# Performance work log

Measured on AMD Instinct MI355X. Metric: run time of the kernel, lower is better.

## Reference

```python
import jax, jax.numpy as jnp
import numpy as np

DIM = 1024
HEADS = 8
HEAD_DIM = DIM // HEADS
D_STATE = 256
BATCH = 8192
DT_MIN = 1e-3
DT_MAX = 1e-1
EPS = 1e-4  # RMSNorm eps


def setup_inputs() -> dict:
    key = jax.random.key(0)
    ks = jax.random.split(key, 8)
    x_t = jax.random.normal(ks[0], (BATCH, DIM), dtype=jnp.float32)
    state_re = jax.random.normal(ks[1], (BATCH, HEADS, D_STATE), dtype=jnp.float32)
    state_im = jax.random.normal(ks[2], (BATCH, HEADS, D_STATE), dtype=jnp.float32)
    # parameters (match torch init)
    norm_weight = jnp.ones((DIM,), dtype=jnp.float32)
    A_re_log = jnp.full((HEADS, D_STATE), float(np.log(0.5)), dtype=jnp.float32)
    n = jnp.arange(1, D_STATE + 1, dtype=jnp.float32)
    A_im = jnp.broadcast_to(float(np.pi) * n, (HEADS, D_STATE)).astype(jnp.float32)
    b_scale = 1.0 / float(np.sqrt(HEAD_DIM))
    c_scale = 1.0 / float(np.sqrt(D_STATE))
    B_re = jax.random.normal(ks[3], (HEADS, D_STATE, HEAD_DIM), dtype=jnp.float32) * b_scale
    B_im = jax.random.normal(ks[4], (HEADS, D_STATE, HEAD_DIM), dtype=jnp.float32) * b_scale
    C_re = jax.random.normal(ks[5], (HEADS, HEAD_DIM, D_STATE), dtype=jnp.float32) * c_scale
    C_im = jax.random.normal(ks[6], (HEADS, HEAD_DIM, D_STATE), dtype=jnp.float32) * c_scale
    D = jnp.ones((DIM,), dtype=jnp.float32)
    # log_dt: inverse-softplus of log-uniform dt in [dt_min, dt_max]
    u = jax.random.uniform(ks[7], (HEADS, D_STATE), dtype=jnp.float32)
    dt = jnp.exp(u * (np.log(DT_MAX) - np.log(DT_MIN)) + np.log(DT_MIN))
    dt = jnp.maximum(dt, 1e-4)
    log_dt = dt + jnp.log(-jnp.expm1(-dt))
    return dict(x_t=x_t, state_re=state_re, state_im=state_im,
                norm_weight=norm_weight, A_re_log=A_re_log, A_im=A_im,
                B_re=B_re, B_im=B_im, C_re=C_re, C_im=C_im, D=D, log_dt=log_dt)


def reference(x_t, state_re, state_im, norm_weight, A_re_log, A_im,
              B_re, B_im, C_re, C_im, D, log_dt):
    batch = x_t.shape[0]
    # RMSNorm (eps=1e-4, elementwise affine)
    ms = jnp.mean(jnp.square(x_t), axis=-1, keepdims=True)
    x = x_t * jax.lax.rsqrt(ms + EPS) * norm_weight
    x_h = x.reshape(batch, HEADS, HEAD_DIM)  # (B,H,P)
    # discretize
    A = jax.lax.complex(-jnp.exp(A_re_log), A_im)            # (H,N)
    dt = jax.nn.softplus(log_dt)                              # (H,N)
    A_bar = jnp.exp(dt.astype(A.dtype) * A)                   # (H,N) complex
    B = jax.lax.complex(B_re, B_im)                           # (H,N,P)
    C = jax.lax.complex(C_re, C_im)                           # (H,P,N)
    B_bar = ((A_bar - 1.0) / A)[..., None] * B                # (H,N,P)
    # recurrent step
    state = jax.lax.complex(state_re, state_im)               # (B,H,N)
    Bx = jnp.einsum('hnp,bhp->bhn', B_bar, x_h.astype(B_bar.dtype))
    new_state = A_bar[None] * state + Bx                      # (B,H,N)
    Ch = jnp.einsum('hpn,bhn->bhp', C, new_state)             # (B,H,P)
    D_h = D.reshape(HEADS, HEAD_DIM)[None]                    # (1,H,P)
    y_h = 2.0 * Ch.real + D_h * x_h
    out = x_t + y_h.reshape(batch, DIM)
    return out, new_state.real, new_state.imag
```

## Files before the change

kernel.cpp:

```cpp
#include <hip/hip_runtime.h>

#define BATCH 8192
#define DIM 1024
#define HEADS 8
#define HEAD_DIM 128
#define DSTATE 256

typedef __attribute__((ext_vector_type(8))) short short8v;
typedef __attribute__((ext_vector_type(4))) float f32x4;
typedef __attribute__((ext_vector_type(4))) unsigned short ushort4v;
typedef __attribute__((ext_vector_type(4))) unsigned int uint4v;

__device__ __forceinline__ unsigned short f2bf(float x) {
  unsigned int u = __builtin_bit_cast(unsigned int, x);
  unsigned int r = u + 0x7FFFu + ((u >> 16) & 1u);
  return (unsigned short)(r >> 16);
}
__device__ __forceinline__ float bf2f(unsigned short h) {
  unsigned int u = ((unsigned int)h) << 16;
  return __builtin_bit_cast(float, u);
}

__device__ __forceinline__ void stage16f(const float* g, float* l) {
  __builtin_amdgcn_global_load_lds(
      (const __attribute__((address_space(1))) unsigned int*)g,
      (__attribute__((address_space(3))) unsigned int*)l, 16, 0, 0);
}
__device__ __forceinline__ void stage16u(const unsigned short* g, unsigned short* l) {
  __builtin_amdgcn_global_load_lds(
      (const __attribute__((address_space(1))) unsigned int*)g,
      (__attribute__((address_space(3))) unsigned int*)l, 16, 0, 0);
}

#define BARRIER() do { \
  asm volatile("s_waitcnt lgkmcnt(0)" ::: "memory"); \
  __builtin_amdgcn_s_barrier(); \
  asm volatile("" ::: "memory"); } while (0)


__global__ void pc_params(const float* __restrict__ logdt,
                          const float* __restrict__ arelog,
                          const float* __restrict__ aim,
                          float* __restrict__ abr, float* __restrict__ abi,
                          float* __restrict__ cre, float* __restrict__ cim) {
  int i = blockIdx.x * 256 + threadIdx.x;
  float ld = logdt[i];
  float dt = log1pf(expf(ld));
  float Ar = -expf(arelog[i]);
  float Ai = aim[i];
  float e  = expf(dt * Ar);
  float th = dt * Ai;
  float Abr = e * cosf(th), Abi = e * sinf(th);
  int n = i & 255, h = i >> 8;
  int s = (n & ~31) + ((n >> 2) & 1) * 16 + ((n >> 3) & 3) * 4 + (n & 3);
  abr[h * 256 + s] = Abr; abi[h * 256 + s] = Abi;
  float den = Ar * Ar + Ai * Ai;
  float br = Abr - 1.0f;
  cre[i] = (br * Ar + Abi * Ai) / den;
  cim[i] = (Abi * Ar - br * Ai) / den;
}

__global__ void pc_w1(const float* __restrict__ Bre, const float* __restrict__ Bim,
                      const float* __restrict__ cre, const float* __restrict__ cim,
                      unsigned short* __restrict__ w1re, unsigned short* __restrict__ w1im) {
  int i = blockIdx.x * 256 + threadIdx.x;
  int p = i & 127, s = (i >> 7) & 255, h = i >> 15;
  int kk = s >> 4, u = s & 15;
  int n = ((kk >> 1) << 5) + ((u >> 2) & 3) * 8 + (kk & 1) * 4 + (u & 3);
  int src = (h * 256 + n) * 128 + p;
  int hn = h * 256 + n;
  float cr = cre[hn], ci = cim[hn];
  float br = Bre[src], bi = Bim[src];
  w1re[i] = f2bf(cr * br - ci * bi);
  w1im[i] = f2bf(cr * bi + ci * br);
}

__global__ void pc_w2(const float* __restrict__ Cre, const float* __restrict__ Cim,
                      unsigned short* __restrict__ w2re, unsigned short* __restrict__ w2mi) {
  int i = blockIdx.x * 256 + threadIdx.x;
  w2re[i] = f2bf(Cre[i]);
  w2mi[i] = f2bf(-Cim[i]);
}

__global__ __launch_bounds__(256) void rms_k(const float* __restrict__ xt,
                                             const float* __restrict__ w,
                                             unsigned short* __restrict__ xbf) {
  int wid = threadIdx.x >> 6, lane = threadIdx.x & 63;
  int row = blockIdx.x * 4 + wid;
  const float* xr = xt + (long)row * DIM;
  f32x4 v[4];
  float ssq = 0.f;
  #pragma unroll
  for (int c = 0; c < 4; ++c) {
    v[c] = *(const f32x4*)(xr + c * 256 + lane * 4);
    ssq += v[c][0]*v[c][0] + v[c][1]*v[c][1] + v[c][2]*v[c][2] + v[c][3]*v[c][3];
  }
  #pragma unroll
  for (int m = 1; m < 64; m <<= 1) ssq += __shfl_xor(ssq, m, 64);
  float sc = rsqrtf(ssq * (1.0f / DIM) + 1e-4f);
  unsigned short* orow = xbf + (long)row * DIM;
  #pragma unroll
  for (int c = 0; c < 4; ++c) {
    f32x4 w4 = *(const f32x4*)(w + c * 256 + lane * 4);
    ushort4v o;
    o[0] = f2bf(v[c][0] * sc * w4[0]);
    o[1] = f2bf(v[c][1] * sc * w4[1]);
    o[2] = f2bf(v[c][2] * sc * w4[2]);
    o[3] = f2bf(v[c][3] * sc * w4[3]);
    *(ushort4v*)(orow + c * 256 + lane * 4) = o;
  }
}

__global__ __launch_bounds__(512, 2) void s5_main(
    const unsigned short* __restrict__ xbf,
    const unsigned short* __restrict__ w1re, const unsigned short* __restrict__ w1im,
    const unsigned short* __restrict__ w2re, const unsigned short* __restrict__ w2mi,
    const float* __restrict__ abrp, const float* __restrict__ abip,
    const float* __restrict__ sre, const float* __restrict__ sim,
    const float* __restrict__ xt, const float* __restrict__ dvec,
    float* __restrict__ out, float* __restrict__ nsre, float* __restrict__ nsim) {
  __shared__ float Sb[3][2][16][256];
  __shared__ float xtl[3][16][128];
  __shared__ unsigned short xbl[3][16][128];
  __shared__ unsigned short pf[2][8][64][8];
  const int tid = threadIdx.x;
  const int w = tid >> 6, lane = tid & 63;
  const int g = lane >> 4, bl = lane & 15;
  const int h = blockIdx.x & 7;
  const int blkrow = (blockIdx.x >> 3) * 256;

  short8v w1r[2][4], w1i[2][4];
  #pragma unroll
  for (int t = 0; t < 2; ++t) {
    const int kk = 2 * w + t;
    const unsigned short* pr = w1re + ((size_t)(h * DSTATE + kk * 16 + bl)) * HEAD_DIM + g * 8;
    const unsigned short* pi = w1im + ((size_t)(h * DSTATE + kk * 16 + bl)) * HEAD_DIM + g * 8;
    #pragma unroll
    for (int ks = 0; ks < 4; ++ks) {
      w1r[t][ks] = *(const short8v*)(pr + ks * 32);
      w1i[t][ks] = *(const short8v*)(pi + ks * 32);
    }
  }
  short8v w2r[8], w2i[8];
  {
    const unsigned short* qr = w2re + ((size_t)(h * HEAD_DIM + w * 16 + bl)) * DSTATE + g * 8;
    const unsigned short* qi = w2mi + ((size_t)(h * HEAD_DIM + w * 16 + bl)) * DSTATE + g * 8;
    #pragma unroll
    for (int j = 0; j < 8; ++j) {
      w2r[j] = *(const short8v*)(qr + j * 32);
      w2i[j] = *(const short8v*)(qi + j * 32);
    }
  }
  f32x4 Arh[2], Aih[2];
  #pragma unroll
  for (int t = 0; t < 2; ++t) {
    Arh[t] = *(const f32x4*)(abrp + h * DSTATE + (2 * w + t) * 16 + g * 4);
    Aih[t] = *(const f32x4*)(abip + h * DSTATE + (2 * w + t) * 16 + g * 4);
  }
  const f32x4 d4 = *(const f32x4*)(dvec + h * HEAD_DIM + w * 16 + g * 4);

  auto STAGE = [&](int t, int b3) {
    const int gr0 = blkrow + t * 16;
    #pragma unroll
    for (int i = 0; i < 2; ++i) {
      const int row = 2 * w + i;
      const size_t rb = ((size_t)(gr0 + row) * HEADS + h) * DSTATE;
      const int soff = (lane ^ (row & 7)) * 4;
      stage16f(sre + rb + soff, &Sb[b3][0][row][0]);
      stage16f(sim + rb + soff, &Sb[b3][1][row][0]);
    }
    {
      const int row = 2 * w + (lane >> 5);
      const float* src = xt + (size_t)(gr0 + row) * DIM + h * HEAD_DIM + (lane & 31) * 4;
      stage16f(src, &xtl[b3][2 * w][0]);
    }
    if (w < 4) {
      const int row = 4 * w + (lane >> 4);
      const unsigned short* src = xbf + (size_t)(gr0 + row) * DIM + h * HEAD_DIM + (lane & 15) * 8;
      stage16u(src, &xbl[b3][4 * w][0]);
    }
  };

  STAGE(0, 0);
  asm volatile("s_waitcnt vmcnt(0)" ::: "memory");
  __builtin_amdgcn_s_barrier();
  asm volatile("" ::: "memory");

  int bcur = 0;
  for (int t = 0; t < 16; ++t) {
    const int bnxt = (bcur == 2) ? 0 : bcur + 1;
    if (t < 15) {
      STAGE(t + 1, bnxt);
      asm volatile("s_waitcnt vmcnt(6)" ::: "memory");
    } else {
      asm volatile("s_waitcnt vmcnt(0)" ::: "memory");
    }
    BARRIER();

    short8v xf[4];
    #pragma unroll
    for (int ks = 0; ks < 4; ++ks)
      xf[ks] = *(const short8v*)&xbl[bcur][bl][ks * 32 + g * 8];

    unsigned pr0 = 0, pr1 = 0, pi0 = 0, pi1 = 0;
    #pragma unroll
    for (int tt = 0; tt < 2; ++tt) {
      f32x4 dr = {0.f,0.f,0.f,0.f};
      f32x4 di = {0.f,0.f,0.f,0.f};
      #pragma unroll
      for (int ks = 0; ks < 4; ++ks)
        dr = __builtin_amdgcn_mfma_f32_16x16x32_bf16(w1r[tt][ks], xf[ks], dr, 0, 0, 0);
      #pragma unroll
      for (int ks = 0; ks < 4; ++ks)
        di = __builtin_amdgcn_mfma_f32_16x16x32_bf16(w1i[tt][ks], xf[ks], di, 0, 0, 0);
      const int c = (((8 * w + 2 * g + tt) ^ (bl & 7)) << 2);
      const f32x4 s_r = *(const f32x4*)&Sb[bcur][0][bl][c];
      const f32x4 s_i = *(const f32x4*)&Sb[bcur][1][bl][c];
      f32x4 nr, ni;
      #pragma unroll
      for (int r = 0; r < 4; ++r) {
        nr[r] = fmaf(Arh[tt][r], s_r[r], fmaf(-Aih[tt][r], s_i[r], dr[r]));
        ni[r] = fmaf(Arh[tt][r], s_i[r], fmaf(Aih[tt][r], s_r[r], di[r]));
      }
      *(f32x4*)&Sb[bcur][0][bl][c] = nr;
      *(f32x4*)&Sb[bcur][1][bl][c] = ni;
      unsigned lo  = (unsigned)f2bf(nr[0]) | ((unsigned)f2bf(nr[1]) << 16);
      unsigned hi  = (unsigned)f2bf(nr[2]) | ((unsigned)f2bf(nr[3]) << 16);
      unsigned lo2 = (unsigned)f2bf(ni[0]) | ((unsigned)f2bf(ni[1]) << 16);
      unsigned hi2 = (unsigned)f2bf(ni[2]) | ((unsigned)f2bf(ni[3]) << 16);
      if (tt == 0) { pr0 = lo; pr1 = hi; pi0 = lo2; pi1 = hi2; }
      else {
        uint4v urv; urv[0] = pr0; urv[1] = pr1; urv[2] = lo;  urv[3] = hi;
        uint4v uiv; uiv[0] = pi0; uiv[1] = pi1; uiv[2] = lo2; uiv[3] = hi2;
        *(short8v*)&pf[0][w][lane][0] = __builtin_bit_cast(short8v, urv);
        *(short8v*)&pf[1][w][lane][0] = __builtin_bit_cast(short8v, uiv);
      }
    }
    BARRIER();

    #pragma unroll
    for (int i = 0; i < 2; ++i) {
      const int row = 2 * w + i;
      const size_t rb = ((size_t)(blkrow + t * 16 + row) * HEADS + h) * DSTATE;
      const int gc = (lane ^ (row & 7)) * 4;
      const f32x4 vr = *(const f32x4*)&Sb[bcur][0][row][lane * 4];
      const f32x4 vi = *(const f32x4*)&Sb[bcur][1][row][lane * 4];
      *(f32x4*)(nsre + rb + gc) = vr;
      *(f32x4*)(nsim + rb + gc) = vi;
    }

    f32x4 a2 = {0.f,0.f,0.f,0.f};
    #pragma unroll
    for (int j = 0; j < 8; ++j) {
      const short8v pbr = *(const short8v*)&pf[0][j][lane][0];
      const short8v pbi = *(const short8v*)&pf[1][j][lane][0];
      a2 = __builtin_amdgcn_mfma_f32_16x16x32_bf16(w2r[j], pbr, a2, 0, 0, 0);
      a2 = __builtin_amdgcn_mfma_f32_16x16x32_bf16(w2i[j], pbi, a2, 0, 0, 0);
    }

    {
      const int col = h * HEAD_DIM + w * 16 + g * 4;
      const size_t o = (size_t)(blkrow + t * 16 + bl) * DIM + col;
      const f32x4 xt4 = *(const f32x4*)&xtl[bcur][bl][w * 16 + g * 4];
      const ushort4v xh4 = *(const ushort4v*)&xbl[bcur][bl][w * 16 + g * 4];
      f32x4 ro;
      #pragma unroll
      for (int r = 0; r < 4; ++r)
        ro[r] = xt4[r] + 2.0f * a2[r] + d4[r] * bf2f(xh4[r]);
      *(f32x4*)(out + o) = ro;
    }
    bcur = bnxt;
  }
}

extern "C" void kernel_launch(void* const* d_in, const int* in_sizes, int n_in,
                              void* d_out, int out_size, void* d_ws, size_t ws_size,
                              hipStream_t stream) {
  const float* x_t      = (const float*)d_in[0];
  const float* state_re = (const float*)d_in[1];
  const float* state_im = (const float*)d_in[2];
  const float* norm_w   = (const float*)d_in[3];
  const float* A_re_log = (const float*)d_in[4];
  const float* A_im     = (const float*)d_in[5];
  const float* B_re     = (const float*)d_in[6];
  const float* B_im     = (const float*)d_in[7];
  const float* C_re     = (const float*)d_in[8];
  const float* C_im     = (const float*)d_in[9];
  const float* Dv       = (const float*)d_in[10];
  const float* log_dt   = (const float*)d_in[11];

  float* out   = (float*)d_out;
  float* ns_re = out + (size_t)BATCH * DIM;
  float* ns_im = ns_re + (size_t)BATCH * HEADS * DSTATE;

  char* ws = (char*)d_ws;
  unsigned short* xbf  = (unsigned short*)ws;
  unsigned short* w1re = (unsigned short*)(ws + 16777216);
  unsigned short* w1im = w1re + 262144;
  unsigned short* w2re = w1im + 262144;
  unsigned short* w2mi = w2re + 262144;
  float* abr = (float*)(ws + 16777216 + 4 * 524288);
  float* abi = abr + 2048;
  float* cre = abi + 2048;
  float* cim = cre + 2048;

  pc_params<<<8, 256, 0, stream>>>(log_dt, A_re_log, A_im, abr, abi, cre, cim);
  pc_w1<<<1024, 256, 0, stream>>>(B_re, B_im, cre, cim, w1re, w1im);
  pc_w2<<<1024, 256, 0, stream>>>(C_re, C_im, w2re, w2mi);
  rms_k<<<2048, 256, 0, stream>>>(x_t, norm_w, xbf);
  s5_main<<<256, 512, 0, stream>>>(xbf, w1re, w1im, w2re, w2mi, abr, abi,
                                   state_re, state_im, x_t, Dv, out, ns_re, ns_im);
}
```

Before: 101.1 us.

## Fuse prep kernels, fold RMSNorm scale into main kernel, deepen staging pipeline

Result: faster. 92.30 us (-8.7%).

```diff
diff --git a/kernel.cpp b/kernel.cpp
--- a/kernel.cpp
+++ b/kernel.cpp
@@ -26,10 +26,10 @@
       (const __attribute__((address_space(1))) unsigned int*)g,
       (__attribute__((address_space(3))) unsigned int*)l, 16, 0, 0);
 }
-__device__ __forceinline__ void stage16u(const unsigned short* g, unsigned short* l) {
+__device__ __forceinline__ void stage4f(const float* g, float* l) {
   __builtin_amdgcn_global_load_lds(
       (const __attribute__((address_space(1))) unsigned int*)g,
-      (__attribute__((address_space(3))) unsigned int*)l, 16, 0, 0);
+      (__attribute__((address_space(3))) unsigned int*)l, 4, 0, 0);
 }
 
 #define BARRIER() do { \
@@ -38,91 +38,72 @@
   asm volatile("" ::: "memory"); } while (0)
 
 
-__global__ void pc_params(const float* __restrict__ logdt,
-                          const float* __restrict__ arelog,
-                          const float* __restrict__ aim,
-                          float* __restrict__ abr, float* __restrict__ abi,
-                          float* __restrict__ cre, float* __restrict__ cim) {
-  int i = blockIdx.x * 256 + threadIdx.x;
-  float ld = logdt[i];
-  float dt = log1pf(expf(ld));
-  float Ar = -expf(arelog[i]);
-  float Ai = aim[i];
-  float e  = expf(dt * Ar);
-  float th = dt * Ai;
-  float Abr = e * cosf(th), Abi = e * sinf(th);
-  int n = i & 255, h = i >> 8;
-  int s = (n & ~31) + ((n >> 2) & 1) * 16 + ((n >> 3) & 3) * 4 + (n & 3);
-  abr[h * 256 + s] = Abr; abi[h * 256 + s] = Abi;
-  float den = Ar * Ar + Ai * Ai;
-  float br = Abr - 1.0f;
-  cre[i] = (br * Ar + Abi * Ai) / den;
-  cim[i] = (Abi * Ar - br * Ai) / den;
-}
-
-__global__ void pc_w1(const float* __restrict__ Bre, const float* __restrict__ Bim,
-                      const float* __restrict__ cre, const float* __restrict__ cim,
-                      unsigned short* __restrict__ w1re, unsigned short* __restrict__ w1im) {
-  int i = blockIdx.x * 256 + threadIdx.x;
-  int p = i & 127, s = (i >> 7) & 255, h = i >> 15;
-  int kk = s >> 4, u = s & 15;
-  int n = ((kk >> 1) << 5) + ((u >> 2) & 3) * 8 + (kk & 1) * 4 + (u & 3);
-  int src = (h * 256 + n) * 128 + p;
-  int hn = h * 256 + n;
-  float cr = cre[hn], ci = cim[hn];
-  float br = Bre[src], bi = Bim[src];
-  w1re[i] = f2bf(cr * br - ci * bi);
-  w1im[i] = f2bf(cr * bi + ci * br);
-}
-
-__global__ void pc_w2(const float* __restrict__ Cre, const float* __restrict__ Cim,
-                      unsigned short* __restrict__ w2re, unsigned short* __restrict__ w2mi) {
-  int i = blockIdx.x * 256 + threadIdx.x;
-  w2re[i] = f2bf(Cre[i]);
-  w2mi[i] = f2bf(-Cim[i]);
-}
-
-__global__ __launch_bounds__(256) void rms_k(const float* __restrict__ xt,
-                                             const float* __restrict__ w,
-                                             unsigned short* __restrict__ xbf) {
-  int wid = threadIdx.x >> 6, lane = threadIdx.x & 63;
-  int row = blockIdx.x * 4 + wid;
-  const float* xr = xt + (long)row * DIM;
-  f32x4 v[4];
-  float ssq = 0.f;
-  #pragma unroll
-  for (int c = 0; c < 4; ++c) {
-    v[c] = *(const f32x4*)(xr + c * 256 + lane * 4);
-    ssq += v[c][0]*v[c][0] + v[c][1]*v[c][1] + v[c][2]*v[c][2] + v[c][3]*v[c][3];
-  }
-  #pragma unroll
-  for (int m = 1; m < 64; m <<= 1) ssq += __shfl_xor(ssq, m, 64);
-  float sc = rsqrtf(ssq * (1.0f / DIM) + 1e-4f);
-  unsigned short* orow = xbf + (long)row * DIM;
-  #pragma unroll
-  for (int c = 0; c < 4; ++c) {
-    f32x4 w4 = *(const f32x4*)(w + c * 256 + lane * 4);
-    ushort4v o;
-    o[0] = f2bf(v[c][0] * sc * w4[0]);
-    o[1] = f2bf(v[c][1] * sc * w4[1]);
-    o[2] = f2bf(v[c][2] * sc * w4[2]);
-    o[3] = f2bf(v[c][3] * sc * w4[3]);
-    *(ushort4v*)(orow + c * 256 + lane * 4) = o;
+__global__ __launch_bounds__(256) void prep(
+    const float* __restrict__ logdt, const float* __restrict__ arelog,
+    const float* __restrict__ aim,
+    const float* __restrict__ Bre, const float* __restrict__ Bim,
+    const float* __restrict__ Cre, const float* __restrict__ Cim,
+    const float* __restrict__ xtg, const float* __restrict__ normw,
+    unsigned short* __restrict__ w1re, unsigned short* __restrict__ w1im,
+    unsigned short* __restrict__ w2re, unsigned short* __restrict__ w2mi,
+    float* __restrict__ abr, float* __restrict__ abi,
+    float* __restrict__ scale) {
+  const int blk = blockIdx.x;
+  if (blk < 1024) {
+    const int i = blk * 256 + threadIdx.x;
+    const int p = i & 127, s = (i >> 7) & 255, h = i >> 15;
+    const int kk = s >> 4, u = s & 15;
+    const int n = ((kk >> 1) << 5) + ((u >> 2) & 3) * 8 + (kk & 1) * 4 + (u & 3);
+    const int hn = h * 256 + n;
+    const float ld = logdt[hn];
+    const float dt = log1pf(expf(ld));
+    const float Ar = -expf(arelog[hn]);
+    const float Ai = aim[hn];
+    const float e = expf(dt * Ar), th = dt * Ai;
+    const float Abr = e * cosf(th), Abi = e * sinf(th);
+    if (p == 0) { abr[h * 256 + s] = Abr; abi[h * 256 + s] = Abi; }
+    const float den = Ar * Ar + Ai * Ai;
+    const float br_ = Abr - 1.0f;
+    const float cr = (br_ * Ar + Abi * Ai) / den;
+    const float ci = (Abi * Ar - br_ * Ai) / den;
+    const int src = hn * 128 + p;
+    const float wb = normw[h * 128 + p];
+    const float bre = Bre[src], bim = Bim[src];
+    w1re[i] = f2bf((cr * bre - ci * bim) * wb);
+    w1im[i] = f2bf((cr * bim + ci * bre) * wb);
+  } else if (blk < 2048) {
+    const int i = (blk - 1024) * 256 + threadIdx.x;
+    w2re[i] = f2bf(Cre[i]);
+    w2mi[i] = f2bf(-Cim[i]);
+  } else {
+    const int wid = threadIdx.x >> 6, lane = threadIdx.x & 63;
+    const int row = (blk - 2048) * 4 + wid;
+    const float* xr = xtg + (size_t)row * DIM;
+    float ssq = 0.f;
+    #pragma unroll
+    for (int c = 0; c < 4; ++c) {
+      const f32x4 v = *(const f32x4*)(xr + c * 256 + lane * 4);
+      ssq += v[0]*v[0] + v[1]*v[1] + v[2]*v[2] + v[3]*v[3];
+    }
+    #pragma unroll
+    for (int m = 1; m < 64; m <<= 1) ssq += __shfl_xor(ssq, m, 64);
+    if (lane == 0) scale[row] = rsqrtf(ssq * (1.0f / DIM) + 1e-4f);
   }
 }
 
 __global__ __launch_bounds__(512, 2) void s5_main(
-    const unsigned short* __restrict__ xbf,
     const unsigned short* __restrict__ w1re, const unsigned short* __restrict__ w1im,
     const unsigned short* __restrict__ w2re, const unsigned short* __restrict__ w2mi,
     const float* __restrict__ abrp, const float* __restrict__ abip,
+    const float* __restrict__ scale,
     const float* __restrict__ sre, const float* __restrict__ sim,
     const float* __restrict__ xt, const float* __restrict__ dvec,
+    const float* __restrict__ normw,
     float* __restrict__ out, float* __restrict__ nsre, float* __restrict__ nsim) {
   __shared__ float Sb[3][2][16][256];
   __shared__ float xtl[3][16][128];
-  __shared__ unsigned short xbl[3][16][128];
   __shared__ unsigned short pf[2][8][64][8];
+  __shared__ float scL[3][64];
   const int tid = threadIdx.x;
   const int w = tid >> 6, lane = tid & 63;
   const int g = lane >> 4, bl = lane & 15;
@@ -157,7 +138,14 @@
     Arh[t] = *(const f32x4*)(abrp + h * DSTATE + (2 * w + t) * 16 + g * 4);
     Aih[t] = *(const f32x4*)(abip + h * DSTATE + (2 * w + t) * 16 + g * 4);
   }
-  const f32x4 d4 = *(const f32x4*)(dvec + h * HEAD_DIM + w * 16 + g * 4);
+  f32x4 d4;
+  {
+    const int col = h * HEAD_DIM + w * 16 + g * 4;
+    const f32x4 dv = *(const f32x4*)(dvec + col);
+    const f32x4 nv = *(const f32x4*)(normw + col);
+    #pragma unroll
+    for (int r = 0; r < 4; ++r) d4[r] = dv[r] * nv[r];
+  }
 
   auto STAGE = [&](int t, int b3) {
     const int gr0 = blkrow + t * 16;
@@ -171,36 +159,37 @@
     }
     {
       const int row = 2 * w + (lane >> 5);
-      const float* src = xt + (size_t)(gr0 + row) * DIM + h * HEAD_DIM + (lane & 31) * 4;
+      const int soff = ((lane & 31) ^ (row & 7)) * 4;
+      const float* src = xt + (size_t)(gr0 + row) * DIM + h * HEAD_DIM + soff;
       stage16f(src, &xtl[b3][2 * w][0]);
     }
-    if (w < 4) {
-      const int row = 4 * w + (lane >> 4);
-      const unsigned short* src = xbf + (size_t)(gr0 + row) * DIM + h * HEAD_DIM + (lane & 15) * 8;
-      stage16u(src, &xbl[b3][4 * w][0]);
-    }
+    stage4f(scale + gr0 + (lane & 15), &scL[b3][0]);
   };
 
   STAGE(0, 0);
-  asm volatile("s_waitcnt vmcnt(0)" ::: "memory");
-  __builtin_amdgcn_s_barrier();
-  asm volatile("" ::: "memory");
-
-  int bcur = 0;
+  STAGE(1, 1);
+
   for (int t = 0; t < 16; ++t) {
-    const int bnxt = (bcur == 2) ? 0 : bcur + 1;
-    if (t < 15) {
-      STAGE(t + 1, bnxt);
-      asm volatile("s_waitcnt vmcnt(6)" ::: "memory");
-    } else {
-      asm volatile("s_waitcnt vmcnt(0)" ::: "memory");
-    }
+    const int bcur = t % 3;
+    if (t < 2) { asm volatile("s_waitcnt vmcnt(6)"  ::: "memory"); }
+    else       { asm volatile("s_waitcnt vmcnt(10)" ::: "memory"); }
     BARRIER();
 
+    if (t + 2 < 16) STAGE(t + 2, (t + 2) % 3);
+
+    const float scl = scL[bcur][bl];
     short8v xf[4];
     #pragma unroll
-    for (int ks = 0; ks < 4; ++ks)
-      xf[ks] = *(const short8v*)&xbl[bcur][bl][ks * 32 + g * 8];
+    for (int ks = 0; ks < 4; ++ks) {
+      const f32x4 x0 = *(const f32x4*)&xtl[bcur][bl][(((ks * 8 + 2 * g)     ^ (bl & 7)) << 2)];
+      const f32x4 x1 = *(const f32x4*)&xtl[bcur][bl][(((ks * 8 + 2 * g + 1) ^ (bl & 7)) << 2)];
+      uint4v uv;
+      uv[0] = (unsigned)f2bf(x0[0] * scl) | ((unsigned)f2bf(x0[1] * scl) << 16);
+      uv[1] = (unsigned)f2bf(x0[2] * scl) | ((unsigned)f2bf(x0[3] * scl) << 16);
+      uv[2] = (unsigned)f2bf(x1[0] * scl) | ((unsigned)f2bf(x1[1] * scl) << 16);
+      uv[3] = (unsigned)f2bf(x1[2] * scl) | ((unsigned)f2bf(x1[3] * scl) << 16);
+      xf[ks] = __builtin_bit_cast(short8v, uv);
+    }
 
     unsigned pr0 = 0, pr1 = 0, pi0 = 0, pi1 = 0;
     #pragma unroll
@@ -261,15 +250,13 @@
     {
       const int col = h * HEAD_DIM + w * 16 + g * 4;
       const size_t o = (size_t)(blkrow + t * 16 + bl) * DIM + col;
-      const f32x4 xt4 = *(const f32x4*)&xtl[bcur][bl][w * 16 + g * 4];
-      const ushort4v xh4 = *(const ushort4v*)&xbl[bcur][bl][w * 16 + g * 4];
+      const f32x4 xt4 = *(const f32x4*)&xtl[bcur][bl][(((4 * w + g) ^ (bl & 7)) << 2)];
       f32x4 ro;
       #pragma unroll
       for (int r = 0; r < 4; ++r)
-        ro[r] = xt4[r] + 2.0f * a2[r] + d4[r] * bf2f(xh4[r]);
+        ro[r] = xt4[r] * (1.0f + d4[r] * scl) + 2.0f * a2[r];
       *(f32x4*)(out + o) = ro;
     }
-    bcur = bnxt;
   }
 }
 
@@ -294,20 +281,18 @@
   float* ns_im = ns_re + (size_t)BATCH * HEADS * DSTATE;
 
   char* ws = (char*)d_ws;
-  unsigned short* xbf  = (unsigned short*)ws;
-  unsigned short* w1re = (unsigned short*)(ws + 16777216);
+  unsigned short* w1re = (unsigned short*)ws;
   unsigned short* w1im = w1re + 262144;
   unsigned short* w2re = w1im + 262144;
   unsigned short* w2mi = w2re + 262144;
-  float* abr = (float*)(ws + 16777216 + 4 * 524288);
-  float* abi = abr + 2048;
-  float* cre = abi + 2048;
-  float* cim = cre + 2048;
-
-  pc_params<<<8, 256, 0, stream>>>(log_dt, A_re_log, A_im, abr, abi, cre, cim);
-  pc_w1<<<1024, 256, 0, stream>>>(B_re, B_im, cre, cim, w1re, w1im);
-  pc_w2<<<1024, 256, 0, stream>>>(C_re, C_im, w2re, w2mi);
-  rms_k<<<2048, 256, 0, stream>>>(x_t, norm_w, xbf);
-  s5_main<<<256, 512, 0, stream>>>(xbf, w1re, w1im, w2re, w2mi, abr, abi,
-                                   state_re, state_im, x_t, Dv, out, ns_re, ns_im);
-}
+  float* abr   = (float*)(ws + 4 * 524288);
+  float* abi   = abr + 2048;
+  float* scale = abi + 2048;
+
+  prep<<<4096, 256, 0, stream>>>(log_dt, A_re_log, A_im, B_re, B_im, C_re, C_im,
+                                 x_t, norm_w, w1re, w1im, w2re, w2mi,
+                                 abr, abi, scale);
+  s5_main<<<256, 512, 0, stream>>>(w1re, w1im, w2re, w2mi, abr, abi, scale,
+                                   state_re, state_im, x_t, Dv, norm_w,
+                                   out, ns_re, ns_im);
+}
```
